# Kernel optimization log

Measured on AMD Instinct MI355X. Metric: run time of the kernel, lower is better.

The kernel has to match this reference:

```python
import jax, jax.numpy as jnp
import numpy as np

B, D, V, T = 256, 1024, 32000, 64  # num_seqs, hidden dim, vocab, history len


def setup_inputs() -> dict:
    key = jax.random.key(0)
    ks = jax.random.split(key, 8)
    hidden = jax.random.normal(ks[0], (B, D), dtype=jnp.float32)
    embedding = jax.random.normal(ks[1], (V, D), dtype=jnp.float32) * (1.0 / np.sqrt(D))
    output_tokens = jax.random.randint(ks[2], (B, T), 0, V, dtype=jnp.int64)
    presence_penalties = jax.random.uniform(ks[3], (B,), dtype=jnp.float32)
    frequency_penalties = jax.random.uniform(ks[4], (B,), dtype=jnp.float32)
    temperatures = jax.random.uniform(ks[5], (B,), dtype=jnp.float32) + 0.5  # > eps
    top_ps = jax.random.uniform(ks[6], (B,), dtype=jnp.float32) * 0.5 + 0.5  # in [0.5, 1.0)
    top_ks = jax.random.randint(ks[7], (B,), 1, V, dtype=jnp.int64)
    return {
        "hidden": hidden,
        "embedding": embedding,
        "output_tokens": output_tokens,
        "presence_penalties": presence_penalties,
        "frequency_penalties": frequency_penalties,
        "temperatures": temperatures,
        "top_ps": top_ps,
        "top_ks": top_ks,
    }


def reference(hidden, embedding, output_tokens, presence_penalties,
              frequency_penalties, temperatures, top_ps, top_ks):
    # 1) logits = pruned hidden states @ embedding^T  -> [B, V]
    logits = jnp.einsum("bd,vd->bv", hidden, embedding)
    b, v = logits.shape

    # 2) presence/frequency penalties via per-row token histogram (np.bincount equiv)
    rows = jnp.broadcast_to(jnp.arange(b)[:, None], output_tokens.shape)
    counts = jnp.zeros((b, v), logits.dtype).at[rows, output_tokens].add(1.0)
    logits = logits - frequency_penalties[:, None] * counts \
                    - presence_penalties[:, None] * (counts > 0).astype(logits.dtype)

    # 3) temperature scaling
    logits = logits / temperatures[:, None]

    # 4) probabilities
    probs = jax.nn.softmax(logits, axis=-1)

    # 5) top-p / top-k: descending sort, cumsum masks, scatter back via inverse perm
    order = jnp.argsort(-probs, axis=-1)                       # descending order
    probs_sort = jnp.take_along_axis(probs, order, axis=-1)
    probs_cum = jnp.cumsum(probs_sort, axis=-1)
    top_p_mask = (probs_cum - probs_sort) > top_ps[:, None]
    top_k_mask = jnp.arange(v)[None, :] >= top_ks[:, None]
    probs_sort = jnp.where(top_p_mask | top_k_mask, 0.0, probs_sort)
    inv = jnp.argsort(order, axis=-1)
    filtered_probs = jnp.take_along_axis(probs_sort, inv, axis=-1)  # original order
    return filtered_probs
```

## Files before the change

### kernel.cpp

```cpp
#include <hip/hip_runtime.h>
#include <math.h>

#define NB 256
#define NV 32000
#define ND 1024
#define NT 64

#define GN 64
#define ASTR 56
#define NKB 64
#define ASLAB (256 * ASTR)
#define NGBLK (NV / GN)
#define INV2048F 4.8828125e-4f

#define NBIN 1024
#define FIX2 4294967296.0
#define PACK1 (1ull << 48)
#define SMASK ((1ull << 48) - 1ull)

typedef _Float16 f16x8 __attribute__((ext_vector_type(8)));
typedef _Float16 f16x4 __attribute__((ext_vector_type(4)));
typedef float f32x16 __attribute__((ext_vector_type(16)));
typedef __attribute__((address_space(3))) void lds_void;
typedef __attribute__((address_space(1))) void glb_void;

struct RowP2 {
  unsigned long long basePack;
  unsigned long long toppZfix;
  unsigned pfx;
  int ktop;
  float invZ;
  unsigned ustar;
  int m;
  int cEq;
};

__device__ __forceinline__ unsigned mono_enc(float f) {
  unsigned u = __float_as_uint(f);
  return (u & 0x80000000u) ? ~u : (u | 0x80000000u);
}
__device__ __forceinline__ float mono_dec(unsigned u) {
  return (u & 0x80000000u) ? __uint_as_float(u & 0x7FFFFFFFu) : __uint_as_float(~u);
}

__global__ __launch_bounds__(256) void convert_A(const float* __restrict__ hidden,
                                                 _Float16* __restrict__ A3) {
  const int kb = blockIdx.x, t = threadIdx.x;
  __shared__ _Float16 slab[ASLAB];
#pragma unroll
  for (int it = 0; it < 4; it++) {
    const int m = it * 64 + (t >> 2);
    const int k4 = (t & 3) * 4;
    float4 a4 = *(const float4*)(hidden + (size_t)m * ND + kb * 16 + k4);
    _Float16* base = slab + m * ASTR;
    float v[4] = {a4.x, a4.y, a4.z, a4.w};
#pragma unroll
    for (int q = 0; q < 4; q++) {
      const _Float16 h = (_Float16)v[q];
      const _Float16 l2 = (_Float16)((v[q] - (float)h) * 2048.0f);
      const int kk = k4 + q;
      base[kk] = h;
      base[16 + 2 * kk] = h;
      base[17 + 2 * kk] = l2;
    }
  }
  __syncthreads();
  const uint4* s = (const uint4*)slab;
  uint4* g = (uint4*)(A3 + (size_t)kb * ASLAB);
#pragma unroll
  for (int i = 0; i < 7; i++) g[i * 256 + t] = s[i * 256 + t];
}

__global__ __launch_bounds__(256, 2) void gemm_f16s(
    const float* __restrict__ Bm, const _Float16* __restrict__ A3,
    const float* __restrict__ temp, unsigned* __restrict__ rowmax,
    float* __restrict__ C) {
  __shared__ _Float16 Als[2][ASLAB];
  __shared__ _Float16 Bls[2][GN * ASTR];
  __shared__ float s_invT[256];
  __shared__ unsigned s_pm[256];

  const int t = threadIdx.x;
  const int l = t & 63, w = t >> 6;
  const int n0 = blockIdx.x * GN;
  s_invT[t] = 1.0f / temp[t];
  s_pm[t] = 0u;

  f32x16 accA[2][2] = {};
  f32x16 accB[2][2] = {};

  const int bn = t >> 2, bk4 = (t & 3) * 4;
  const int l31 = l & 31, lh = l >> 5;
  const int ka = lh * 8;
  const int mb = w * 64;

  const float* browp = Bm + (size_t)(n0 + bn) * ND + bk4;
  const char* gaBase = (const char*)A3 + (w * 7) * 1024 + l * 16;
  char* laB0 = (char*)&Als[0][0] + (w * 7) * 1024;
  char* laB1 = (char*)&Als[1][0] + (w * 7) * 1024;

#define ISSUE_A(kbn, LA)                                                        \
  do {                                                                          \
    const char* ga_ = gaBase + (size_t)(kbn) * (ASLAB * 2);                     \
    _Pragma("unroll") for (int i_ = 0; i_ < 7; i_++)                            \
        __builtin_amdgcn_global_load_lds((const glb_void*)(ga_ + i_ * 1024),    \
                                         (lds_void*)((LA) + i_ * 1024), 16, 0,  \
                                         0);                                    \
  } while (0)

#define BCONV(BV, DST)                                                          \
  do {                                                                          \
    const _Float16 h0_ = (_Float16)(BV).x, h1_ = (_Float16)(BV).y,              \
                   h2_ = (_Float16)(BV).z, h3_ = (_Float16)(BV).w;              \
    const _Float16 q0_ = (_Float16)(((BV).x - (float)h0_) * 2048.0f);           \
    const _Float16 q1_ = (_Float16)(((BV).y - (float)h1_) * 2048.0f);           \
    const _Float16 q2_ = (_Float16)(((BV).z - (float)h2_) * 2048.0f);           \
    const _Float16 q3_ = (_Float16)(((BV).w - (float)h3_) * 2048.0f);           \
    _Float16* prow_ = (DST) + bn * ASTR;                                        \
    *(f16x4*)(prow_ + bk4) = (f16x4){h0_, h1_, h2_, h3_};                       \
    *(f16x8*)(prow_ + 16 + 2 * bk4) =                                           \
        (f16x8){q0_, h0_, q1_, h1_, q2_, h2_, q3_, h3_};                        \
  } while (0)

#define COMPUTE(CUR)                                                                       \
  do {                                                                                     \
    const _Float16* Ap_ = &Als[CUR][0] + (size_t)(mb + l31) * ASTR + ka;                   \
    const _Float16* Bp_ = &Bls[CUR][0] + (size_t)l31 * ASTR + ka;                          \
    f16x8 a0_ = *(const f16x8*)(Ap_);                                                      \
    f16x8 a1_ = *(const f16x8*)(Ap_ + 32 * ASTR);                                          \
    f16x8 b0_ = *(const f16x8*)(Bp_);                                                      \
    f16x8 b1_ = *(const f16x8*)(Bp_ + 32 * ASTR);                                          \
    accA[0][0] = __builtin_amdgcn_mfma_f32_32x32x16_f16(a0_, b0_, accA[0][0], 0, 0, 0);    \
    accA[0][1] = __builtin_amdgcn_mfma_f32_32x32x16_f16(a0_, b1_, accA[0][1], 0, 0, 0);    \
    accA[1][0] = __builtin_amdgcn_mfma_f32_32x32x16_f16(a1_, b0_, accA[1][0], 0, 0, 0);    \
    accA[1][1] = __builtin_amdgcn_mfma_f32_32x32x16_f16(a1_, b1_, accA[1][1], 0, 0, 0);    \
    _Pragma("unroll") for (int s_ = 0; s_ < 2; s_++) {                                     \
      const int off_ = 16 + s_ * 16;                                                       \
      f16x8 c0_ = *(const f16x8*)(Ap_ + off_);                                             \
      f16x8 c1_ = *(const f16x8*)(Ap_ + 32 * ASTR + off_);                                 \
      f16x8 d0_ = *(const f16x8*)(Bp_ + off_);                                             \
      f16x8 d1_ = *(const f16x8*)(Bp_ + 32 * ASTR + off_);                                 \
      accB[0][0] = __builtin_amdgcn_mfma_f32_32x32x16_f16(c0_, d0_, accB[0][0], 0, 0, 0);  \
      accB[0][1] = __builtin_amdgcn_mfma_f32_32x32x16_f16(c0_, d1_, accB[0][1], 0, 0, 0);  \
      accB[1][0] = __builtin_amdgcn_mfma_f32_32x32x16_f16(c1_, d0_, accB[1][0], 0, 0, 0);  \
      accB[1][1] = __builtin_amdgcn_mfma_f32_32x32x16_f16(c1_, d1_, accB[1][1], 0, 0, 0);  \
    }                                                                                      \
  } while (0)

  ISSUE_A(0, laB0);
  __builtin_amdgcn_sched_barrier(0);
  float4 bv0 = *(const float4*)(browp);
  __builtin_amdgcn_sched_barrier(0);
  float4 bvA = *(const float4*)(browp + 16);
  __builtin_amdgcn_sched_barrier(0);
  asm volatile("s_waitcnt vmcnt(1)" ::: "memory");
  BCONV(bv0, &Bls[0][0]);
  asm volatile("s_waitcnt lgkmcnt(0)\ns_barrier" ::: "memory");

  float4 bvB;
  for (int kb = 0; kb < 62; kb += 2) {
    ISSUE_A(kb + 1, laB1);
    __builtin_amdgcn_sched_barrier(0);
    bvB = *(const float4*)(browp + (size_t)(kb + 2) * 16);
    __builtin_amdgcn_sched_barrier(0);
    asm volatile("s_waitcnt vmcnt(9)" ::: "memory");
    COMPUTE(0);
    __builtin_amdgcn_sched_barrier(0);
    asm volatile("s_waitcnt vmcnt(8)" ::: "memory");
    BCONV(bvA, &Bls[1][0]);
    asm volatile("s_waitcnt lgkmcnt(0)\ns_barrier" ::: "memory");

    ISSUE_A(kb + 2, laB0);
    __builtin_amdgcn_sched_barrier(0);
    bvA = *(const float4*)(browp + (size_t)(kb + 3) * 16);
    __builtin_amdgcn_sched_barrier(0);
    asm volatile("s_waitcnt vmcnt(9)" ::: "memory");
    COMPUTE(1);
    __builtin_amdgcn_sched_barrier(0);
    asm volatile("s_waitcnt vmcnt(8)" ::: "memory");
    BCONV(bvB, &Bls[0][0]);
    asm volatile("s_waitcnt lgkmcnt(0)\ns_barrier" ::: "memory");
  }

  ISSUE_A(63, laB1);
  __builtin_amdgcn_sched_barrier(0);
  asm volatile("s_waitcnt vmcnt(8)" ::: "memory");
  COMPUTE(0);
  __builtin_amdgcn_sched_barrier(0);
  asm volatile("s_waitcnt vmcnt(7)" ::: "memory");
  BCONV(bvA, &Bls[1][0]);
  asm volatile("s_waitcnt lgkmcnt(0)\ns_barrier" ::: "memory");

  asm volatile("s_waitcnt vmcnt(0)" ::: "memory");
  COMPUTE(1);

#undef ISSUE_A
#undef BCONV
#undef COMPUTE

#pragma unroll
  for (int mi = 0; mi < 2; mi++) {
#pragma unroll
    for (int r = 0; r < 16; r++) {
      const int row = mb + mi * 32 + (r & 3) + 8 * (r >> 2) + 4 * lh;
      const float it = s_invT[row];
      float v0 = (accA[mi][0][r] + accB[mi][0][r] * INV2048F) * it;
      float v1 = (accA[mi][1][r] + accB[mi][1][r] * INV2048F) * it;
      C[(size_t)row * NV + n0 + l31] = v0;
      C[(size_t)row * NV + n0 + 32 + l31] = v1;
      float mx = fmaxf(v0, v1);
#pragma unroll
      for (int o = 1; o < 32; o <<= 1) mx = fmaxf(mx, __shfl_xor(mx, o));
      if (l31 == 0) atomicMax(&s_pm[row], mono_enc(mx));
    }
  }
  __syncthreads();
  atomicMax(&rowmax[t], s_pm[t]);
}

__global__ __launch_bounds__(64) void s0_prep(
    const unsigned* __restrict__ rowmax, const int* __restrict__ toks,
    const float* __restrict__ pres, const float* __restrict__ freq,
    const float* __restrict__ temp, float* __restrict__ Mrow,
    float* __restrict__ buf) {
  const int b = blockIdx.x, t = threadIdx.x;
  __shared__ int s_tok[NT];
  s_tok[t] = toks[b * NT + t];
  __syncthreads();
  const int tk = s_tok[t];
  bool first = true; int cnt = 0;
  for (int j = 0; j < NT; j++)
    if (s_tok[j] == tk) { if (j < t) first = false; cnt++; }
  if (first)
    buf[(size_t)b * NV + tk] -= (freq[b] * (float)cnt + pres[b]) / temp[b];
  if (t == 0) Mrow[b] = mono_dec(rowmax[b]);
}

__global__ __launch_bounds__(256) void h_l0(
    float* __restrict__ buf, const float* __restrict__ Mrow,
    unsigned long long* __restrict__ histP) {
  const int b = blockIdx.x >> 3, sl = blockIdx.x & 7, t = threadIdx.x;
  __shared__ unsigned long long h[NBIN];
  for (int i = t; i < NBIN; i += 256) h[i] = 0ull;
  __syncthreads();
  const float M = Mrow[b];
  float* row = buf + (size_t)b * NV;
  const int base = sl * 4096;
#pragma unroll
  for (int it = 0; it < 4; it++) {
    const int idx = base + (it * 256 + t) * 4;
    if (idx < NV) {
      float4 x4 = *(const float4*)(row + idx);
      float4 e4;
      e4.x = expf(x4.x - M); e4.y = expf(x4.y - M);
      e4.z = expf(x4.z - M); e4.w = expf(x4.w - M);
      *(float4*)(row + idx) = e4;
      unsigned k;
      k = __float_as_uint(e4.x); if (k) atomicAdd(&h[k >> 20], PACK1 | (unsigned long long)(e4.x * FIX2));
      k = __float_as_uint(e4.y); if (k) atomicAdd(&h[k >> 20], PACK1 | (unsigned long long)(e4.y * FIX2));
      k = __float_as_uint(e4.z); if (k) atomicAdd(&h[k >> 20], PACK1 | (unsigned long long)(e4.z * FIX2));
      k = __float_as_uint(e4.w); if (k) atomicAdd(&h[k >> 20], PACK1 | (unsigned long long)(e4.w * FIX2));
    }
  }
  __syncthreads();
  unsigned long long* gh = histP + (size_t)b * NBIN;
  for (int i = t; i < NBIN; i += 256)
    if (h[i]) atomicAdd(&gh[i], h[i]);
}

__global__ __launch_bounds__(256) void h_ref(
    const float* __restrict__ buf, const RowP2* __restrict__ params,
    unsigned long long* __restrict__ histP, int matchShift, int binShift) {
  const int b = blockIdx.x >> 3, sl = blockIdx.x & 7, t = threadIdx.x;
  __shared__ unsigned long long h[NBIN];
  for (int i = t; i < NBIN; i += 256) h[i] = 0ull;
  __syncthreads();
  const unsigned pfx = params[b].pfx;
  const float* row = buf + (size_t)b * NV;
  const int base = sl * 4096;
#pragma unroll
  for (int it = 0; it < 4; it++) {
    const int idx = base + (it * 256 + t) * 4;
    if (idx < NV) {
      float4 e4 = *(const float4*)(row + idx);
      unsigned k;
      k = __float_as_uint(e4.x); if (k && (k >> matchShift) == pfx) atomicAdd(&h[(k >> binShift) & 1023u], PACK1 | (unsigned long long)(e4.x * FIX2));
      k = __float_as_uint(e4.y); if (k && (k >> matchShift) == pfx) atomicAdd(&h[(k >> binShift) & 1023u], PACK1 | (unsigned long long)(e4.y * FIX2));
      k = __float_as_uint(e4.z); if (k && (k >> matchShift) == pfx) atomicAdd(&h[(k >> binShift) & 1023u], PACK1 | (unsigned long long)(e4.z * FIX2));
      k = __float_as_uint(e4.w); if (k && (k >> matchShift) == pfx) atomicAdd(&h[(k >> binShift) & 1023u], PACK1 | (unsigned long long)(e4.w * FIX2));
    }
  }
  __syncthreads();
  unsigned long long* gh = histP + (size_t)b * NBIN;
  for (int i = t; i < NBIN; i += 256)
    if (h[i]) atomicAdd(&gh[i], h[i]);
}

__global__ __launch_bounds__(256) void s2_level(
    unsigned long long* __restrict__ histP, const float* __restrict__ topp_a,
    const int* __restrict__ topk_a, RowP2* __restrict__ params, int level) {
  const int b = blockIdx.x, t = threadIdx.x;
  __shared__ unsigned long long suf[NBIN];
  __shared__ unsigned long long sc[256];
  __shared__ int s_bs;
  unsigned long long* hp = histP + (size_t)b * NBIN;
  unsigned long long v[4];
#pragma unroll
  for (int i = 0; i < 4; i++) { v[i] = hp[t * 4 + i]; hp[t * 4 + i] = 0ull; }
  if (t == 0) s_bs = 1023;
  sc[t] = v[0] + v[1] + v[2] + v[3];
  __syncthreads();
  for (int off = 1; off < 256; off <<= 1) {
    unsigned long long add = (t + off < 256) ? sc[t + off] : 0ull;
    __syncthreads();
    sc[t] += add;
    __syncthreads();
  }
  const unsigned long long totalP = sc[0];
  unsigned long long run = (t < 255) ? sc[t + 1] : 0ull;
  suf[t * 4 + 3] = run; run += v[3];
  suf[t * 4 + 2] = run; run += v[2];
  suf[t * 4 + 1] = run; run += v[1];
  suf[t * 4 + 0] = run;
  __syncthreads();

  RowP2 p;
  unsigned long long base, toppZ;
  int ktop_;
  if (level == 0) {
    ktop_ = topk_a[b];
    unsigned long long Zfix = totalP & SMASK;
    if (!Zfix) Zfix = 1ull;
    toppZ = (unsigned long long)((double)topp_a[b] * (double)Zfix);
    base = 0ull;
    p.pfx = 0; p.invZ = (float)(FIX2 / (double)Zfix);
    p.ustar = 0; p.m = 0; p.cEq = 0;
  } else {
    p = params[b];
    base = p.basePack; toppZ = p.toppZfix; ktop_ = p.ktop;
  }

#pragma unroll
  for (int i = 0; i < 4; i++) {
    const int bin = t * 4 + i;
    const unsigned long long sG = base + suf[bin];
    const bool A = ((long long)(sG >> 48) < (long long)ktop_) && ((sG & SMASK) <= toppZ);
    const unsigned long long sPfull = base + ((bin > 0) ? suf[bin - 1] : totalP);
    const bool Ap = ((long long)(sPfull >> 48) < (long long)ktop_) && ((sPfull & SMASK) <= toppZ);
    if (A && !Ap) s_bs = bin;
  }
  __syncthreads();
  if (t == 0) {
    const int bs = s_bs;
    const unsigned long long newBase = base + suf[bs];
    if (level < 2) {
      p.basePack = newBase;
      p.toppZfix = toppZ;
      p.ktop = ktop_;
      p.pfx = (level == 0) ? (unsigned)bs : ((p.pfx << 10) | (unsigned)bs);
      params[b] = p;
    } else {
      const unsigned ustar = (p.pfx << 10) | (unsigned)bs;
      const unsigned long long raw = ((bs > 0) ? suf[bs - 1] : totalP) - suf[bs];
      const int cEq = (int)(raw >> 48);
      const long long Chi = (long long)(newBase >> 48);
      const unsigned long long Shi = newBase & SMASK;
      long long m = cEq;
      const long long lim = (long long)ktop_ - Chi;
      if (lim < m) m = lim;
      const double tf = (double)__uint_as_float(ustar) * FIX2;
      const double rem = (double)(toppZ - Shi);
      const double Rd = floor(rem / tf) + 1.0;
      if (Rd < (double)m) m = (long long)Rd;
      if (m < 1) m = 1;
      p.ustar = ustar; p.m = (int)m; p.cEq = cEq;
      params[b] = p;
    }
  }
}

__global__ __launch_bounds__(256) void s3_filter(
    float* __restrict__ buf, const RowP2* __restrict__ params) {
  const int b = blockIdx.x >> 3, sl = blockIdx.x & 7, t = threadIdx.x;
  const RowP2 p = params[b];
  const unsigned ustar = p.ustar;
  const float invZ = p.invZ;
  const bool need = (p.m < p.cEq);
  float* row = buf + (size_t)b * NV;
  const int base = sl * 4096;
#pragma unroll
  for (int it = 0; it < 4; it++) {
    const int idx = base + (it * 256 + t) * 4;
    if (idx < NV) {
      float4 e4 = *(const float4*)(row + idx);
      float4 o4;
      unsigned k;
      k = __float_as_uint(e4.x);
      o4.x = (k > ustar) ? e4.x * invZ : ((k == ustar) ? (need ? -e4.x : e4.x * invZ) : 0.f);
      k = __float_as_uint(e4.y);
      o4.y = (k > ustar) ? e4.y * invZ : ((k == ustar) ? (need ? -e4.y : e4.y * invZ) : 0.f);
      k = __float_as_uint(e4.z);
      o4.z = (k > ustar) ? e4.z * invZ : ((k == ustar) ? (need ? -e4.z : e4.z * invZ) : 0.f);
      k = __float_as_uint(e4.w);
      o4.w = (k > ustar) ? e4.w * invZ : ((k == ustar) ? (need ? -e4.w : e4.w * invZ) : 0.f);
      *(float4*)(row + idx) = o4;
    }
  }
}

__global__ __launch_bounds__(256) void s5_tie(
    float* __restrict__ buf, const RowP2* __restrict__ params) {
  const int b = blockIdx.x, t = threadIdx.x;
  const RowP2 p = params[b];
  if (p.m >= p.cEq) return;
  const int m = p.m;
  const float invZ = p.invZ;
  float* row = buf + (size_t)b * NV;
  __shared__ int s_rank[256];
  const int CH = NV / 256;
  const int base = t * CH, end = base + CH;
  int myc = 0;
  for (int v = base; v < end; v++) myc += (row[v] < 0.f);
  s_rank[t] = myc;
  __syncthreads();
  for (int off = 1; off < 256; off <<= 1) {
    const int v0 = s_rank[t];
    const int vn = (t >= off) ? s_rank[t - off] : 0;
    __syncthreads();
    s_rank[t] = v0 + vn;
    __syncthreads();
  }
  int r = (t > 0) ? s_rank[t - 1] : 0;
  for (int v = base; v < end; v++) {
    const float f = row[v];
    if (f < 0.f) {
      row[v] = (r < m) ? (-f) * invZ : 0.f;
      r++;
    }
  }
}

extern "C" void kernel_launch(void* const* d_in, const int* in_sizes, int n_in,
                              void* d_out, int out_size, void* d_ws, size_t ws_size,
                              hipStream_t stream) {
  (void)in_sizes; (void)n_in; (void)out_size; (void)ws_size;
  const float* hidden = (const float*)d_in[0];
  const float* emb    = (const float*)d_in[1];
  const int*   toks   = (const int*)d_in[2];
  const float* pres   = (const float*)d_in[3];
  const float* freq   = (const float*)d_in[4];
  const float* temp   = (const float*)d_in[5];
  const float* topp   = (const float*)d_in[6];
  const int*   topk   = (const int*)d_in[7];
  float* out = (float*)d_out;

  const size_t offA3   = 0;
  const size_t offRM   = 1835008;
  const size_t offHist = offRM + 1024;
  const size_t offMr   = offHist + 2097152;
  const size_t offPar  = offMr + 1024;

  _Float16* A3 = (_Float16*)((char*)d_ws + offA3);
  unsigned* rowmax = (unsigned*)((char*)d_ws + offRM);
  unsigned long long* histP = (unsigned long long*)((char*)d_ws + offHist);
  float* Mrow = (float*)((char*)d_ws + offMr);
  RowP2* params = (RowP2*)((char*)d_ws + offPar);

  hipMemsetAsync((char*)d_ws + offRM, 0, 1024 + 2097152, stream);
  convert_A<<<NKB, 256, 0, stream>>>(hidden, A3);
  gemm_f16s<<<NGBLK, 256, 0, stream>>>(emb, A3, temp, rowmax, out);
  s0_prep<<<NB, 64, 0, stream>>>(rowmax, toks, pres, freq, temp, Mrow, out);
  h_l0<<<NB * 8, 256, 0, stream>>>(out, Mrow, histP);
  s2_level<<<NB, 256, 0, stream>>>(histP, topp, topk, params, 0);
  h_ref<<<NB * 8, 256, 0, stream>>>(out, params, histP, 20, 10);
  s2_level<<<NB, 256, 0, stream>>>(histP, topp, topk, params, 1);
  h_ref<<<NB * 8, 256, 0, stream>>>(out, params, histP, 10, 0);
  s2_level<<<NB, 256, 0, stream>>>(histP, topp, topk, params, 2);
  s3_filter<<<NB * 8, 256, 0, stream>>>(out, params);
  s5_tie<<<NB, 256, 0, stream>>>(out, params);
}
```

Measured before the change: 319.5 us.

## Fuse post-GEMM sampling pipeline into one LDS-resident per-row kernel

Replaces the nine post-GEMM launches (penalty prep, three histogram passes, three level scans, filter, tie fix) with a single kernel, one block per row. The kernel stages the 32000-float row in about 136 KB of dynamic LDS and runs every radix-select level on that copy. This removes repeated global reads and writes of the logits, the global histogram atomics, the large memset and the launch gaps. In exchange, parallelism drops from 2048 blocks to 256 one-per-row blocks with large LDS, which caps occupancy at one block per CU and leaves each row on a single CU.

```diff
diff --git a/kernel.cpp b/kernel.cpp
--- a/kernel.cpp
+++ b/kernel.cpp
@@ -17,6 +17,7 @@
 #define FIX2 4294967296.0
 #define PACK1 (1ull << 48)
 #define SMASK ((1ull << 48) - 1ull)
+#define SMEM_BYTES (NV * 4 + NBIN * 8)
 
 typedef _Float16 f16x8 __attribute__((ext_vector_type(8)));
 typedef _Float16 f16x4 __attribute__((ext_vector_type(4)));
@@ -218,224 +219,179 @@
   atomicMax(&rowmax[t], s_pm[t]);
 }
 
-__global__ __launch_bounds__(64) void s0_prep(
-    const unsigned* __restrict__ rowmax, const int* __restrict__ toks,
-    const float* __restrict__ pres, const float* __restrict__ freq,
-    const float* __restrict__ temp, float* __restrict__ Mrow,
-    float* __restrict__ buf) {
+__global__ __launch_bounds__(256) void sample_row(
+    float* __restrict__ buf, const unsigned* __restrict__ rowmax,
+    const int* __restrict__ toks, const float* __restrict__ pres,
+    const float* __restrict__ freq, const float* __restrict__ temp,
+    const float* __restrict__ topp_a, const int* __restrict__ topk_a) {
+  extern __shared__ char smem[];
+  float* e = (float*)smem;
+  unsigned long long* h = (unsigned long long*)(smem + NV * 4);
+  __shared__ unsigned long long sc[256];
+  __shared__ int s_rank[256];
+  __shared__ int s_tok[NT];
+  __shared__ int s_bs;
+  __shared__ RowP2 sp;
+
   const int b = blockIdx.x, t = threadIdx.x;
-  __shared__ int s_tok[NT];
-  s_tok[t] = toks[b * NT + t];
+  float* row = buf + (size_t)b * NV;
+
+  if (t < NT) s_tok[t] = toks[b * NT + t];
+  for (int i = t; i < NBIN; i += 256) h[i] = 0ull;
+  for (int i4 = t; i4 < NV / 4; i4 += 256)
+    *(float4*)(e + i4 * 4) = *(const float4*)(row + i4 * 4);
   __syncthreads();
-  const int tk = s_tok[t];
-  bool first = true; int cnt = 0;
-  for (int j = 0; j < NT; j++)
-    if (s_tok[j] == tk) { if (j < t) first = false; cnt++; }
-  if (first)
-    buf[(size_t)b * NV + tk] -= (freq[b] * (float)cnt + pres[b]) / temp[b];
-  if (t == 0) Mrow[b] = mono_dec(rowmax[b]);
-}
-
-__global__ __launch_bounds__(256) void h_l0(
-    float* __restrict__ buf, const float* __restrict__ Mrow,
-    unsigned long long* __restrict__ histP) {
-  const int b = blockIdx.x >> 3, sl = blockIdx.x & 7, t = threadIdx.x;
-  __shared__ unsigned long long h[NBIN];
-  for (int i = t; i < NBIN; i += 256) h[i] = 0ull;
+
+  if (t < NT) {
+    const int tk = s_tok[t];
+    bool first = true; int cnt = 0;
+    for (int j = 0; j < NT; j++)
+      if (s_tok[j] == tk) { if (j < t) first = false; cnt++; }
+    if (first) e[tk] -= (freq[b] * (float)cnt + pres[b]) / temp[b];
+  }
   __syncthreads();
-  const float M = Mrow[b];
-  float* row = buf + (size_t)b * NV;
-  const int base = sl * 4096;
-#pragma unroll
-  for (int it = 0; it < 4; it++) {
-    const int idx = base + (it * 256 + t) * 4;
-    if (idx < NV) {
-      float4 x4 = *(const float4*)(row + idx);
-      float4 e4;
-      e4.x = expf(x4.x - M); e4.y = expf(x4.y - M);
-      e4.z = expf(x4.z - M); e4.w = expf(x4.w - M);
-      *(float4*)(row + idx) = e4;
-      unsigned k;
-      k = __float_as_uint(e4.x); if (k) atomicAdd(&h[k >> 20], PACK1 | (unsigned long long)(e4.x * FIX2));
-      k = __float_as_uint(e4.y); if (k) atomicAdd(&h[k >> 20], PACK1 | (unsigned long long)(e4.y * FIX2));
-      k = __float_as_uint(e4.z); if (k) atomicAdd(&h[k >> 20], PACK1 | (unsigned long long)(e4.z * FIX2));
-      k = __float_as_uint(e4.w); if (k) atomicAdd(&h[k >> 20], PACK1 | (unsigned long long)(e4.w * FIX2));
-    }
+
+  const float M = mono_dec(rowmax[b]);
+  for (int i4 = t; i4 < NV / 4; i4 += 256) {
+    float4 x4 = *(const float4*)(e + i4 * 4);
+    float4 e4;
+    e4.x = expf(x4.x - M); e4.y = expf(x4.y - M);
+    e4.z = expf(x4.z - M); e4.w = expf(x4.w - M);
+    *(float4*)(e + i4 * 4) = e4;
+    unsigned k;
+    k = __float_as_uint(e4.x); if (k) atomicAdd(&h[k >> 20], PACK1 | (unsigned long long)(e4.x * FIX2));
+    k = __float_as_uint(e4.y); if (k) atomicAdd(&h[k >> 20], PACK1 | (unsigned long long)(e4.y * FIX2));
+    k = __float_as_uint(e4.z); if (k) atomicAdd(&h[k >> 20], PACK1 | (unsigned long long)(e4.z * FIX2));
+    k = __float_as_uint(e4.w); if (k) atomicAdd(&h[k >> 20], PACK1 | (unsigned long long)(e4.w * FIX2));
   }
   __syncthreads();
-  unsigned long long* gh = histP + (size_t)b * NBIN;
-  for (int i = t; i < NBIN; i += 256)
-    if (h[i]) atomicAdd(&gh[i], h[i]);
-}
-
-__global__ __launch_bounds__(256) void h_ref(
-    const float* __restrict__ buf, const RowP2* __restrict__ params,
-    unsigned long long* __restrict__ histP, int matchShift, int binShift) {
-  const int b = blockIdx.x >> 3, sl = blockIdx.x & 7, t = threadIdx.x;
-  __shared__ unsigned long long h[NBIN];
-  for (int i = t; i < NBIN; i += 256) h[i] = 0ull;
-  __syncthreads();
-  const unsigned pfx = params[b].pfx;
-  const float* row = buf + (size_t)b * NV;
-  const int base = sl * 4096;
-#pragma unroll
-  for (int it = 0; it < 4; it++) {
-    const int idx = base + (it * 256 + t) * 4;
-    if (idx < NV) {
-      float4 e4 = *(const float4*)(row + idx);
-      unsigned k;
-      k = __float_as_uint(e4.x); if (k && (k >> matchShift) == pfx) atomicAdd(&h[(k >> binShift) & 1023u], PACK1 | (unsigned long long)(e4.x * FIX2));
-      k = __float_as_uint(e4.y); if (k && (k >> matchShift) == pfx) atomicAdd(&h[(k >> binShift) & 1023u], PACK1 | (unsigned long long)(e4.y * FIX2));
-      k = __float_as_uint(e4.z); if (k && (k >> matchShift) == pfx) atomicAdd(&h[(k >> binShift) & 1023u], PACK1 | (unsigned long long)(e4.z * FIX2));
-      k = __float_as_uint(e4.w); if (k && (k >> matchShift) == pfx) atomicAdd(&h[(k >> binShift) & 1023u], PACK1 | (unsigned long long)(e4.w * FIX2));
-    }
-  }
-  __syncthreads();
-  unsigned long long* gh = histP + (size_t)b * NBIN;
-  for (int i = t; i < NBIN; i += 256)
-    if (h[i]) atomicAdd(&gh[i], h[i]);
-}
-
-__global__ __launch_bounds__(256) void s2_level(
-    unsigned long long* __restrict__ histP, const float* __restrict__ topp_a,
-    const int* __restrict__ topk_a, RowP2* __restrict__ params, int level) {
-  const int b = blockIdx.x, t = threadIdx.x;
-  __shared__ unsigned long long suf[NBIN];
-  __shared__ unsigned long long sc[256];
-  __shared__ int s_bs;
-  unsigned long long* hp = histP + (size_t)b * NBIN;
-  unsigned long long v[4];
-#pragma unroll
-  for (int i = 0; i < 4; i++) { v[i] = hp[t * 4 + i]; hp[t * 4 + i] = 0ull; }
-  if (t == 0) s_bs = 1023;
-  sc[t] = v[0] + v[1] + v[2] + v[3];
-  __syncthreads();
-  for (int off = 1; off < 256; off <<= 1) {
-    unsigned long long add = (t + off < 256) ? sc[t + off] : 0ull;
+
+  for (int level = 0; level < 3; level++) {
+    unsigned long long v0 = h[t * 4], v1 = h[t * 4 + 1],
+                       v2 = h[t * 4 + 2], v3 = h[t * 4 + 3];
+    if (t == 0) s_bs = 1023;
+    sc[t] = v0 + v1 + v2 + v3;
     __syncthreads();
-    sc[t] += add;
+    for (int off = 1; off < 256; off <<= 1) {
+      unsigned long long add = (t + off < 256) ? sc[t + off] : 0ull;
+      __syncthreads();
+      sc[t] += add;
+      __syncthreads();
+    }
+    const unsigned long long totalP = sc[0];
+    unsigned long long run = (t < 255) ? sc[t + 1] : 0ull;
+    h[t * 4 + 3] = run; run += v3;
+    h[t * 4 + 2] = run; run += v2;
+    h[t * 4 + 1] = run; run += v1;
+    h[t * 4 + 0] = run;
     __syncthreads();
-  }
-  const unsigned long long totalP = sc[0];
-  unsigned long long run = (t < 255) ? sc[t + 1] : 0ull;
-  suf[t * 4 + 3] = run; run += v[3];
-  suf[t * 4 + 2] = run; run += v[2];
-  suf[t * 4 + 1] = run; run += v[1];
-  suf[t * 4 + 0] = run;
-  __syncthreads();
-
-  RowP2 p;
-  unsigned long long base, toppZ;
-  int ktop_;
-  if (level == 0) {
-    ktop_ = topk_a[b];
-    unsigned long long Zfix = totalP & SMASK;
-    if (!Zfix) Zfix = 1ull;
-    toppZ = (unsigned long long)((double)topp_a[b] * (double)Zfix);
-    base = 0ull;
-    p.pfx = 0; p.invZ = (float)(FIX2 / (double)Zfix);
-    p.ustar = 0; p.m = 0; p.cEq = 0;
-  } else {
-    p = params[b];
-    base = p.basePack; toppZ = p.toppZfix; ktop_ = p.ktop;
-  }
-
-#pragma unroll
-  for (int i = 0; i < 4; i++) {
-    const int bin = t * 4 + i;
-    const unsigned long long sG = base + suf[bin];
-    const bool A = ((long long)(sG >> 48) < (long long)ktop_) && ((sG & SMASK) <= toppZ);
-    const unsigned long long sPfull = base + ((bin > 0) ? suf[bin - 1] : totalP);
-    const bool Ap = ((long long)(sPfull >> 48) < (long long)ktop_) && ((sPfull & SMASK) <= toppZ);
-    if (A && !Ap) s_bs = bin;
-  }
-  __syncthreads();
-  if (t == 0) {
-    const int bs = s_bs;
-    const unsigned long long newBase = base + suf[bs];
+
+    unsigned long long base, toppZ;
+    int ktop_;
+    if (level == 0) {
+      ktop_ = topk_a[b];
+      unsigned long long Zfix = totalP & SMASK;
+      if (!Zfix) Zfix = 1ull;
+      toppZ = (unsigned long long)((double)topp_a[b] * (double)Zfix);
+      base = 0ull;
+    } else {
+      base = sp.basePack; toppZ = sp.toppZfix; ktop_ = sp.ktop;
+    }
+
+#pragma unroll
+    for (int i = 0; i < 4; i++) {
+      const int bin = t * 4 + i;
+      const unsigned long long sG = base + h[bin];
+      const bool A = ((long long)(sG >> 48) < (long long)ktop_) && ((sG & SMASK) <= toppZ);
+      const unsigned long long sPfull = base + ((bin > 0) ? h[bin - 1] : totalP);
+      const bool Ap = ((long long)(sPfull >> 48) < (long long)ktop_) && ((sPfull & SMASK) <= toppZ);
+      if (A && !Ap) s_bs = bin;
+    }
+    __syncthreads();
+    if (t == 0) {
+      const int bs = s_bs;
+      const unsigned long long newBase = base + h[bs];
+      if (level == 0) {
+        unsigned long long Zfix = totalP & SMASK;
+        if (!Zfix) Zfix = 1ull;
+        sp.invZ = (float)(FIX2 / (double)Zfix);
+      }
+      if (level < 2) {
+        sp.basePack = newBase;
+        sp.toppZfix = toppZ;
+        sp.ktop = ktop_;
+        sp.pfx = (level == 0) ? (unsigned)bs : ((sp.pfx << 10) | (unsigned)bs);
+      } else {
+        const unsigned ustar = (sp.pfx << 10) | (unsigned)bs;
+        const unsigned long long raw = ((bs > 0) ? h[bs - 1] : totalP) - h[bs];
+        const int cEq = (int)(raw >> 48);
+        const long long Chi = (long long)(newBase >> 48);
+        const unsigned long long Shi = newBase & SMASK;
+        long long m = cEq;
+        const long long lim = (long long)ktop_ - Chi;
+        if (lim < m) m = lim;
+        const double tf = (double)__uint_as_float(ustar) * FIX2;
+        const double rem = (double)(toppZ - Shi);
+        const double Rd = floor(rem / tf) + 1.0;
+        if (Rd < (double)m) m = (long long)Rd;
+        if (m < 1) m = 1;
+        sp.ustar = ustar; sp.m = (int)m; sp.cEq = cEq;
+      }
+    }
+    __syncthreads();
     if (level < 2) {
-      p.basePack = newBase;
-      p.toppZfix = toppZ;
-      p.ktop = ktop_;
-      p.pfx = (level == 0) ? (unsigned)bs : ((p.pfx << 10) | (unsigned)bs);
-      params[b] = p;
-    } else {
-      const unsigned ustar = (p.pfx << 10) | (unsigned)bs;
-      const unsigned long long raw = ((bs > 0) ? suf[bs - 1] : totalP) - suf[bs];
-      const int cEq = (int)(raw >> 48);
-      const long long Chi = (long long)(newBase >> 48);
-      const unsigned long long Shi = newBase & SMASK;
-      long long m = cEq;
-      const long long lim = (long long)ktop_ - Chi;
-      if (lim < m) m = lim;
-      const double tf = (double)__uint_as_float(ustar) * FIX2;
-      const double rem = (double)(toppZ - Shi);
-      const double Rd = floor(rem / tf) + 1.0;
-      if (Rd < (double)m) m = (long long)Rd;
-      if (m < 1) m = 1;
-      p.ustar = ustar; p.m = (int)m; p.cEq = cEq;
-      params[b] = p;
-    }
-  }
-}
-
-__global__ __launch_bounds__(256) void s3_filter(
-    float* __restrict__ buf, const RowP2* __restrict__ params) {
-  const int b = blockIdx.x >> 3, sl = blockIdx.x & 7, t = threadIdx.x;
-  const RowP2 p = params[b];
-  const unsigned ustar = p.ustar;
-  const float invZ = p.invZ;
-  const bool need = (p.m < p.cEq);
-  float* row = buf + (size_t)b * NV;
-  const int base = sl * 4096;
-#pragma unroll
-  for (int it = 0; it < 4; it++) {
-    const int idx = base + (it * 256 + t) * 4;
-    if (idx < NV) {
-      float4 e4 = *(const float4*)(row + idx);
+      for (int i = t; i < NBIN; i += 256) h[i] = 0ull;
+      __syncthreads();
+      const unsigned pfx = sp.pfx;
+      const int ms = (level == 0) ? 20 : 10;
+      const int bsh = (level == 0) ? 10 : 0;
+      for (int i4 = t; i4 < NV / 4; i4 += 256) {
+        float4 e4 = *(const float4*)(e + i4 * 4);
+        unsigned k;
+        k = __float_as_uint(e4.x); if (k && (k >> ms) == pfx) atomicAdd(&h[(k >> bsh) & 1023u], PACK1 | (unsigned long long)(e4.x * FIX2));
+        k = __float_as_uint(e4.y); if (k && (k >> ms) == pfx) atomicAdd(&h[(k >> bsh) & 1023u], PACK1 | (unsigned long long)(e4.y * FIX2));
+        k = __float_as_uint(e4.z); if (k && (k >> ms) == pfx) atomicAdd(&h[(k >> bsh) & 1023u], PACK1 | (unsigned long long)(e4.z * FIX2));
+        k = __float_as_uint(e4.w); if (k && (k >> ms) == pfx) atomicAdd(&h[(k >> bsh) & 1023u], PACK1 | (unsigned long long)(e4.w * FIX2));
+      }
+      __syncthreads();
+    }
+  }
+
+  const unsigned ustar = sp.ustar;
+  const float invZ = sp.invZ;
+  if (sp.m >= sp.cEq) {
+    for (int i4 = t; i4 < NV / 4; i4 += 256) {
+      float4 e4 = *(const float4*)(e + i4 * 4);
       float4 o4;
       unsigned k;
-      k = __float_as_uint(e4.x);
-      o4.x = (k > ustar) ? e4.x * invZ : ((k == ustar) ? (need ? -e4.x : e4.x * invZ) : 0.f);
-      k = __float_as_uint(e4.y);
-      o4.y = (k > ustar) ? e4.y * invZ : ((k == ustar) ? (need ? -e4.y : e4.y * invZ) : 0.f);
-      k = __float_as_uint(e4.z);
-      o4.z = (k > ustar) ? e4.z * invZ : ((k == ustar) ? (need ? -e4.z : e4.z * invZ) : 0.f);
-      k = __float_as_uint(e4.w);
-      o4.w = (k > ustar) ? e4.w * invZ : ((k == ustar) ? (need ? -e4.w : e4.w * invZ) : 0.f);
-      *(float4*)(row + idx) = o4;
-    }
-  }
-}
-
-__global__ __launch_bounds__(256) void s5_tie(
-    float* __restrict__ buf, const RowP2* __restrict__ params) {
-  const int b = blockIdx.x, t = threadIdx.x;
-  const RowP2 p = params[b];
-  if (p.m >= p.cEq) return;
-  const int m = p.m;
-  const float invZ = p.invZ;
-  float* row = buf + (size_t)b * NV;
-  __shared__ int s_rank[256];
-  const int CH = NV / 256;
-  const int base = t * CH, end = base + CH;
-  int myc = 0;
-  for (int v = base; v < end; v++) myc += (row[v] < 0.f);
-  s_rank[t] = myc;
-  __syncthreads();
-  for (int off = 1; off < 256; off <<= 1) {
-    const int v0 = s_rank[t];
-    const int vn = (t >= off) ? s_rank[t - off] : 0;
+      k = __float_as_uint(e4.x); o4.x = (k >= ustar) ? e4.x * invZ : 0.f;
+      k = __float_as_uint(e4.y); o4.y = (k >= ustar) ? e4.y * invZ : 0.f;
+      k = __float_as_uint(e4.z); o4.z = (k >= ustar) ? e4.z * invZ : 0.f;
+      k = __float_as_uint(e4.w); o4.w = (k >= ustar) ? e4.w * invZ : 0.f;
+      *(float4*)(row + i4 * 4) = o4;
+    }
+  } else {
+    const int m = sp.m;
+    const int CH = NV / 256;
+    const int base0 = t * CH;
+    int myc = 0;
+    for (int v = base0; v < base0 + CH; v++)
+      myc += (__float_as_uint(e[v]) == ustar);
+    s_rank[t] = myc;
     __syncthreads();
-    s_rank[t] = v0 + vn;
-    __syncthreads();
-  }
-  int r = (t > 0) ? s_rank[t - 1] : 0;
-  for (int v = base; v < end; v++) {
-    const float f = row[v];
-    if (f < 0.f) {
-      row[v] = (r < m) ? (-f) * invZ : 0.f;
-      r++;
+    for (int off = 1; off < 256; off <<= 1) {
+      const int a0 = s_rank[t];
+      const int an = (t >= off) ? s_rank[t - off] : 0;
+      __syncthreads();
+      s_rank[t] = a0 + an;
+      __syncthreads();
+    }
+    int r = (t > 0) ? s_rank[t - 1] : 0;
+    for (int v = base0; v < base0 + CH; v++) {
+      const unsigned k = __float_as_uint(e[v]);
+      float o = (k > ustar) ? e[v] * invZ : 0.f;
+      if (k == ustar) { o = (r < m) ? e[v] * invZ : 0.f; r++; }
+      row[v] = o;
     }
   }
 }
@@ -454,28 +410,18 @@
   const int*   topk   = (const int*)d_in[7];
   float* out = (float*)d_out;
 
-  const size_t offA3   = 0;
-  const size_t offRM   = 1835008;
-  const size_t offHist = offRM + 1024;
-  const size_t offMr   = offHist + 2097152;
-  const size_t offPar  = offMr + 1024;
+  const size_t offA3 = 0;
+  const size_t offRM = 1835008;
 
   _Float16* A3 = (_Float16*)((char*)d_ws + offA3);
   unsigned* rowmax = (unsigned*)((char*)d_ws + offRM);
-  unsigned long long* histP = (unsigned long long*)((char*)d_ws + offHist);
-  float* Mrow = (float*)((char*)d_ws + offMr);
-  RowP2* params = (RowP2*)((char*)d_ws + offPar);
-
-  hipMemsetAsync((char*)d_ws + offRM, 0, 1024 + 2097152, stream);
+
+  hipFuncSetAttribute((const void*)sample_row,
+                      hipFuncAttributeMaxDynamicSharedMemorySize, SMEM_BYTES);
+
+  hipMemsetAsync((char*)d_ws + offRM, 0, 1024, stream);
   convert_A<<<NKB, 256, 0, stream>>>(hidden, A3);
   gemm_f16s<<<NGBLK, 256, 0, stream>>>(emb, A3, temp, rowmax, out);
-  s0_prep<<<NB, 64, 0, stream>>>(rowmax, toks, pres, freq, temp, Mrow, out);
-  h_l0<<<NB * 8, 256, 0, stream>>>(out, Mrow, histP);
-  s2_level<<<NB, 256, 0, stream>>>(histP, topp, topk, params, 0);
-  h_ref<<<NB * 8, 256, 0, stream>>>(out, params, histP, 20, 10);
-  s2_level<<<NB, 256, 0, stream>>>(histP, topp, topk, params, 1);
-  h_ref<<<NB * 8, 256, 0, stream>>>(out, params, histP, 10, 0);
-  s2_level<<<NB, 256, 0, stream>>>(histP, topp, topk, params, 2);
-  s3_filter<<<NB * 8, 256, 0, stream>>>(out, params);
-  s5_tie<<<NB, 256, 0, stream>>>(out, params);
-}
+  sample_row<<<NB, 256, SMEM_BYTES, stream>>>(out, rowmax, toks, pres, freq,
+                                              temp, topp, topk);
+}
```

Result: no change. 324.2 us (+1.5%).
